# Optimization experiments

Measured on AMD Instinct MI355X. Metric: run time of the kernel, lower is better.

The kernel has to match this reference:

```python
import jax, jax.numpy as jnp
import numpy as np

# Sizes
N, T, P, D = 1000, 4, 10, 13          # nodes, point types, edge types (T*(T+1)/2), basis dim per point
F, H, EA, K, E = 128, 128, 16, 64, 20000  # node feat, edge hidden, edge attr/feat, edge op bottleneck, edges
I_NODE = D * (D + 1) // 2             # 91: symmetric ('ij=ji') self-block irreps dim
I_EDGE = D * D                        # 169: generic ('ij') block irreps dim
AVG_NEIGH = 20.0


def setup_inputs() -> dict:
    ks = jax.random.split(jax.random.key(0), 16)
    Fin = H + 2 * F                   # edge-op input: [edge_msg, node_h_i, node_h_j]
    return {
        'node_feats': jax.random.normal(ks[0], (N, F), jnp.float32),
        'node_attrs': jax.random.uniform(ks[1], (N, T), dtype=jnp.float32),
        'edge_feats': jax.random.normal(ks[2], (E, EA), jnp.float32),
        'edge_attrs': jax.random.normal(ks[3], (E, EA), jnp.float32),
        'edge_index': jax.random.randint(ks[4], (2, E), 0, N),
        'node_types': jax.random.randint(ks[5], (N,), 0, T),
        'edge_types': jax.random.randint(ks[6], (E,), 0, P),
        'W_msg': jax.random.normal(ks[7], (F, F), jnp.float32) / np.float32(np.sqrt(F)),
        'W_attr': jax.random.normal(ks[8], (T, F), jnp.float32) / np.float32(np.sqrt(T)),
        'W_em': jax.random.normal(ks[9], (2 * F + 2 * EA, H), jnp.float32) / np.float32(np.sqrt(2 * F + 2 * EA)),
        'W_proj': jax.random.normal(ks[10], (Fin, K), jnp.float32) / np.float32(np.sqrt(Fin)),
        'W_node': jax.random.normal(ks[11], (T, F, I_NODE), jnp.float32) / np.float32(np.sqrt(F)),
        'W_edge': jax.random.normal(ks[12], (P, K, I_EDGE), jnp.float32) / np.float32(np.sqrt(K)),
        'cob_node': jax.random.normal(ks[13], (T, I_NODE, D, D), jnp.float32) / np.float32(D),
        'cob_edge': jax.random.normal(ks[14], (P, I_EDGE, D, D), jnp.float32) / np.float32(D),
    }


def reference(node_feats, node_attrs, edge_feats, edge_attrs, edge_index, node_types,
              edge_types, W_msg, W_attr, W_em, W_proj, W_node, W_edge, cob_node, cob_edge):
    src, dst = edge_index[0], edge_index[1]
    # --- node message passing (NodeMessageBlock, simplified linear-aggregate form) ---
    m = node_feats @ W_msg                                             # [N, F]
    agg = jax.ops.segment_sum(m[src], dst, num_segments=N) \
        + jax.ops.segment_sum(m[dst], src, num_segments=N)             # symmetric edge list: both dirs
    node_h = node_feats + agg / AVG_NEIGH + node_attrs @ W_attr        # [N, F]
    # --- edge messages (EdgeMessageBlock, simplified) ---
    e_in = jnp.concatenate([node_h[src], node_h[dst], edge_feats, edge_attrs], axis=-1)
    edge_msg = jnp.tanh(e_in @ W_em)                                   # [E, H]
    # --- self-interaction blocks: per-type gather -> op -> einsum('ni,ixy->nxy', ., cob) ---
    node_irred = jnp.einsum('nf,nfi->ni', node_h, W_node[node_types])  # [N, I_NODE]
    node_blocks = jnp.einsum('ni,nixy->nxy', node_irred, cob_node[node_types])  # [N, D, D]
    # --- interaction blocks: per-edge-type op + change of basis, transpose-symmetrized ---
    onehot = jax.nn.one_hot(edge_types, P, dtype=node_feats.dtype)     # [E, P] type selector

    def edge_block(a, b):
        h = jnp.concatenate([edge_msg, a, b], axis=-1) @ W_proj        # [E, K]
        irr = jnp.einsum('epi,ep->ei', jnp.einsum('ek,pki->epi', h, W_edge), onehot)  # [E, I_EDGE]
        return jnp.einsum('epxy,ep->exy', jnp.einsum('ei,pixy->epxy', irr, cob_edge), onehot)  # [E, D, D]

    blk_ij = edge_block(node_h[src], node_h[dst])
    blk_ji = edge_block(node_h[dst], node_h[src])
    edge_blocks = 0.5 * (blk_ij + jnp.swapaxes(blk_ji, -1, -2))        # symm_transpose
    # --- scatter blocks into the dense symmetric block matrix ---
    off = jnp.arange(D)
    nidx = jnp.arange(N)[:, None] * D + off                            # [N, D] diagonal block rows/cols
    rs = src[:, None] * D + off                                        # [E, D]
    cs = dst[:, None] * D + off
    M = jnp.zeros((N * D, N * D), node_feats.dtype)
    M = M.at[nidx[:, :, None], nidx[:, None, :]].add(node_blocks)
    M = M.at[rs[:, :, None], cs[:, None, :]].add(edge_blocks)
    M = M.at[cs[:, :, None], rs[:, None, :]].add(jnp.swapaxes(edge_blocks, -1, -2))
    return M
```

## Files before the change

### kernel.cpp

```cpp
#include <hip/hip_runtime.h>
#include <cmath>

#define NN   1000
#define TT   4
#define PP   10
#define DD   13
#define FF   128
#define HH   128
#define EAA  16
#define KDIM 64
#define EE   20000
#define I_NODE 91
#define I_EDGE 169
#define MROW  13000
#define OUT_FLOAT4 42250000L

__global__ __launch_bounds__(256) void k_zero(float4* __restrict__ p, long n4) {
  long i = (long)blockIdx.x * 256 + threadIdx.x;
  if (i < n4) p[i] = make_float4(0.f, 0.f, 0.f, 0.f);
}

__global__ __launch_bounds__(192) void k_comb_edge(
    const float* __restrict__ We, const float* __restrict__ cob,
    float* __restrict__ Wcomb) {
  int pk = blockIdx.x;
  int p = pk >> 6;
  int t = threadIdx.x;
  if (t >= I_EDGE) return;
  float acc = 0.f;
  const float* wrow = We + pk * I_EDGE;
  const float* crow = cob + p * I_EDGE * I_EDGE + t;
  for (int i = 0; i < I_EDGE; ++i) acc += wrow[i] * crow[i * I_EDGE];
  Wcomb[pk * I_EDGE + t] = acc;
}

__global__ __launch_bounds__(192) void k_comb_node(
    const float* __restrict__ Wn, const float* __restrict__ cob,
    float* __restrict__ Wnc) {
  int tf = blockIdx.x;
  int ty = tf >> 7;
  int t = threadIdx.x;
  if (t >= I_EDGE) return;
  float acc = 0.f;
  const float* wrow = Wn + tf * I_NODE;
  const float* crow = cob + ty * I_NODE * I_EDGE + t;
  for (int i = 0; i < I_NODE; ++i) acc += wrow[i] * crow[i * I_EDGE];
  Wnc[tf * I_EDGE + t] = acc;
}

__global__ __launch_bounds__(128) void k_node_msg(
    const float* __restrict__ nf, const float* __restrict__ Wmsg,
    float* __restrict__ m, float* __restrict__ agg) {
  int n = blockIdx.x, j = threadIdx.x;
  __shared__ float row[FF];
  row[j] = nf[n * FF + j];
  __syncthreads();
  float acc = 0.f;
#pragma unroll 8
  for (int f = 0; f < FF; ++f) acc += row[f] * Wmsg[f * FF + j];
  m[n * FF + j] = acc;
  agg[n * FF + j] = 0.f;
}

__global__ __launch_bounds__(256) void k_scatter(
    const float* __restrict__ m, const int* __restrict__ src,
    const int* __restrict__ dst, float* __restrict__ agg) {
  int idx = blockIdx.x * 256 + threadIdx.x;
  if (idx >= EE * FF) return;
  int e = idx >> 7, j = idx & 127;
  int s = src[e], d = dst[e];
  atomicAdd(&agg[d * FF + j], m[s * FF + j]);
  atomicAdd(&agg[s * FF + j], m[d * FF + j]);
}

__global__ __launch_bounds__(128) void k_node_h(
    const float* __restrict__ nf, const float* __restrict__ agg,
    const float* __restrict__ na, const float* __restrict__ Wattr,
    float* __restrict__ nh) {
  int n = blockIdx.x, j = threadIdx.x;
  float a = 0.f;
#pragma unroll
  for (int t = 0; t < TT; ++t) a += na[n * TT + t] * Wattr[t * FF + j];
  nh[n * FF + j] = nf[n * FF + j] + agg[n * FF + j] * (1.0f / 20.0f) + a;
}

__global__ __launch_bounds__(128) void k_node_pre(
    const float* __restrict__ nh, const float* __restrict__ Wem,
    const float* __restrict__ Wproj, float* __restrict__ V1,
    float* __restrict__ V2, float* __restrict__ U) {
  int n = blockIdx.x, t = threadIdx.x;
  __shared__ float row[FF];
  row[t] = nh[n * FF + t];
  __syncthreads();
  float v1 = 0.f, v2 = 0.f;
#pragma unroll 4
  for (int f = 0; f < FF; ++f) {
    float x = row[f];
    v1 += x * Wem[f * HH + t];
    v2 += x * Wem[(FF + f) * HH + t];
  }
  V1[n * HH + t] = v1;
  V2[n * HH + t] = v2;
  int k = t & 63, half = t >> 6;
  const float* W = Wproj + (FF + half * FF) * KDIM + k;
  float u = 0.f;
#pragma unroll 4
  for (int f = 0; f < FF; ++f) u += row[f] * W[f * KDIM];
  U[n * 128 + t] = u;
}

#define EPB 8
__global__ __launch_bounds__(128) void k_edge_msg(
    const float* __restrict__ V1, const float* __restrict__ V2,
    const float* __restrict__ ef, const float* __restrict__ ea,
    const int* __restrict__ src, const int* __restrict__ dst,
    const float* __restrict__ Wem, const float* __restrict__ Wproj,
    float* __restrict__ hmsg) {
  int e0 = blockIdx.x * EPB;
  int j = threadIdx.x;
  __shared__ float efa[EPB][32];
  __shared__ float em[EPB][HH];
  for (int i = j; i < EPB * 32; i += 128) {
    int e = i >> 5, c = i & 31;
    efa[e][c] = (c < 16) ? ef[(e0 + e) * EAA + c] : ea[(e0 + e) * EAA + (c - 16)];
  }
  __syncthreads();
  float wcol[32];
#pragma unroll
  for (int c = 0; c < 32; ++c) wcol[c] = Wem[(256 + c) * HH + j];
#pragma unroll
  for (int e = 0; e < EPB; ++e) {
    int s = src[e0 + e], d = dst[e0 + e];
    float acc = V1[s * HH + j] + V2[d * HH + j];
#pragma unroll
    for (int c = 0; c < 32; ++c) acc += efa[e][c] * wcol[c];
    em[e][j] = tanhf(acc);
  }
  __syncthreads();
  int k = j & 63, half = j >> 6;
  float a0 = 0.f, a1 = 0.f, a2 = 0.f, a3 = 0.f;
  for (int f = 0; f < HH; f += 4) {
    float4 m0 = *(const float4*)&em[half + 0][f];
    float4 m1 = *(const float4*)&em[half + 2][f];
    float4 m2 = *(const float4*)&em[half + 4][f];
    float4 m3 = *(const float4*)&em[half + 6][f];
    float w0 = Wproj[(f + 0) * KDIM + k], w1 = Wproj[(f + 1) * KDIM + k];
    float w2 = Wproj[(f + 2) * KDIM + k], w3 = Wproj[(f + 3) * KDIM + k];
    a0 += m0.x * w0 + m0.y * w1 + m0.z * w2 + m0.w * w3;
    a1 += m1.x * w0 + m1.y * w1 + m1.z * w2 + m1.w * w3;
    a2 += m2.x * w0 + m2.y * w1 + m2.z * w2 + m2.w * w3;
    a3 += m3.x * w0 + m3.y * w1 + m3.z * w2 + m3.w * w3;
  }
  hmsg[(e0 + half + 0) * KDIM + k] = a0;
  hmsg[(e0 + half + 2) * KDIM + k] = a1;
  hmsg[(e0 + half + 4) * KDIM + k] = a2;
  hmsg[(e0 + half + 6) * KDIM + k] = a3;
}

__global__ __launch_bounds__(192) void k_node_block(
    const float* __restrict__ nh, const int* __restrict__ ntype,
    const float* __restrict__ Wnc, float* __restrict__ M) {
  int n = blockIdx.x, t = threadIdx.x;
  int ty = ntype[n];
  __shared__ float row[FF];
  if (t < FF) row[t] = nh[n * FF + t];
  __syncthreads();
  if (t < I_EDGE) {
    float acc = 0.f;
    const float* W = Wnc + ty * FF * I_EDGE + t;
#pragma unroll 4
    for (int f = 0; f < FF; ++f) acc += row[f] * W[f * I_EDGE];
    int x = t / DD, y = t % DD;
    atomicAdd(&M[(size_t)(n * DD + x) * MROW + (n * DD + y)], acc);
  }
}

#define EB2 4
__global__ __launch_bounds__(768) void k_edge_blk(
    const float* __restrict__ U, const float* __restrict__ hmsg,
    const int* __restrict__ src, const int* __restrict__ dst,
    const int* __restrict__ etype, const float* __restrict__ Wcomb,
    float* __restrict__ M) {
  int e0 = blockIdx.x * EB2;
  int t = threadIdx.x;
  int ei = threadIdx.y;
  int e = e0 + ei;
  __shared__ float h[EB2][2][KDIM];
  __shared__ float tji[EB2][I_EDGE];
  int s = src[e], d = dst[e], p = etype[e];
  if (t < 128) {
    int k = t & 63, w = t >> 6;
    int a = w ? d : s, b = w ? s : d;
    h[ei][w][k] = hmsg[e * KDIM + k] + U[a * 128 + k] + U[b * 128 + 64 + k];
  }
  __syncthreads();
  float bij = 0.f, bji = 0.f;
  if (t < I_EDGE) {
    const float* W = Wcomb + p * KDIM * I_EDGE + t;
    for (int k = 0; k < KDIM; k += 4) {
      float4 hi = *(const float4*)&h[ei][0][k];
      float4 hj = *(const float4*)&h[ei][1][k];
      float w0 = W[(k + 0) * I_EDGE], w1 = W[(k + 1) * I_EDGE];
      float w2 = W[(k + 2) * I_EDGE], w3 = W[(k + 3) * I_EDGE];
      bij += hi.x * w0 + hi.y * w1 + hi.z * w2 + hi.w * w3;
      bji += hj.x * w0 + hj.y * w1 + hj.z * w2 + hj.w * w3;
    }
    tji[ei][t] = bji;
  }
  __syncthreads();
  if (t < I_EDGE) {
    int x = t / DD, y = t % DD;
    float eb = 0.5f * (bij + tji[ei][y * DD + x]);
    atomicAdd(&M[(size_t)(s * DD + x) * MROW + (d * DD + y)], eb);
    atomicAdd(&M[(size_t)(d * DD + y) * MROW + (s * DD + x)], eb);
  }
}

extern "C" void kernel_launch(void* const* d_in, const int* in_sizes, int n_in,
                              void* d_out, int out_size, void* d_ws, size_t ws_size,
                              hipStream_t stream) {
  const float* node_feats = (const float*)d_in[0];
  const float* node_attrs = (const float*)d_in[1];
  const float* edge_feats = (const float*)d_in[2];
  const float* edge_attrs = (const float*)d_in[3];
  const int*   edge_index = (const int*)d_in[4];
  const int*   node_types = (const int*)d_in[5];
  const int*   edge_types = (const int*)d_in[6];
  const float* W_msg  = (const float*)d_in[7];
  const float* W_attr = (const float*)d_in[8];
  const float* W_em   = (const float*)d_in[9];
  const float* W_proj = (const float*)d_in[10];
  const float* W_node = (const float*)d_in[11];
  const float* W_edge = (const float*)d_in[12];
  const float* cob_node = (const float*)d_in[13];
  const float* cob_edge = (const float*)d_in[14];

  float* M  = (float*)d_out;
  float* ws = (float*)d_ws;
  float* m_buf = ws;
  float* agg   = ws + 128000;
  float* nh    = ws + 256000;
  float* V1    = ws + 384000;
  float* V2    = ws + 512000;
  float* U     = ws + 640000;
  float* hmsg  = ws + 768000;
  float* Wcomb = ws + 2048000;
  float* Wnc   = ws + 2156160;

  const int* src = edge_index;
  const int* dst = edge_index + EE;

  k_zero      <<<(int)((OUT_FLOAT4 + 255) / 256), 256, 0, stream>>>((float4*)M, OUT_FLOAT4);
  k_comb_edge <<<PP * KDIM, 192, 0, stream>>>(W_edge, cob_edge, Wcomb);
  k_comb_node <<<TT * FF, 192, 0, stream>>>(W_node, cob_node, Wnc);
  k_node_msg  <<<NN, 128, 0, stream>>>(node_feats, W_msg, m_buf, agg);
  k_scatter   <<<(EE * FF) / 256, 256, 0, stream>>>(m_buf, src, dst, agg);
  k_node_h    <<<NN, 128, 0, stream>>>(node_feats, agg, node_attrs, W_attr, nh);
  k_node_pre  <<<NN, 128, 0, stream>>>(nh, W_em, W_proj, V1, V2, U);
  k_edge_msg  <<<EE / EPB, 128, 0, stream>>>(V1, V2, edge_feats, edge_attrs, src, dst,
                                             W_em, W_proj, hmsg);
  k_node_block<<<NN, 192, 0, stream>>>(nh, node_types, Wnc, M);
  k_edge_blk  <<<dim3(EE / EB2), dim3(192, 4), 0, stream>>>(U, hmsg, src, dst, edge_types,
                                                            Wcomb, M);
}
```

Measured before the change: 892.5 us.

## Fuse setup, node, and edge stages into fewer kernels

Merges the zero-fill, weight-combination and node message kernels into one heterogeneous front kernel that dispatches on block index. The node-h, node-pre and node-block kernels become one per-node kernel, and the edge message MLP moves into the edge-block kernel so the hmsg intermediate is never written to global memory. This cuts launch count and intermediate traffic. In exchange, the edge kernel now recomputes the projection per edge with fewer threads active in its early phases and no register-cached weights.

```diff
diff --git a/kernel.cpp b/kernel.cpp
--- a/kernel.cpp
+++ b/kernel.cpp
@@ -15,51 +15,57 @@
 #define MROW  13000
 #define OUT_FLOAT4 42250000L
 
-__global__ __launch_bounds__(256) void k_zero(float4* __restrict__ p, long n4) {
-  long i = (long)blockIdx.x * 256 + threadIdx.x;
-  if (i < n4) p[i] = make_float4(0.f, 0.f, 0.f, 0.f);
-}
-
-__global__ __launch_bounds__(192) void k_comb_edge(
-    const float* __restrict__ We, const float* __restrict__ cob,
-    float* __restrict__ Wcomb) {
-  int pk = blockIdx.x;
-  int p = pk >> 6;
-  int t = threadIdx.x;
-  if (t >= I_EDGE) return;
-  float acc = 0.f;
-  const float* wrow = We + pk * I_EDGE;
-  const float* crow = cob + p * I_EDGE * I_EDGE + t;
-  for (int i = 0; i < I_EDGE; ++i) acc += wrow[i] * crow[i * I_EDGE];
-  Wcomb[pk * I_EDGE + t] = acc;
-}
-
-__global__ __launch_bounds__(192) void k_comb_node(
-    const float* __restrict__ Wn, const float* __restrict__ cob,
-    float* __restrict__ Wnc) {
-  int tf = blockIdx.x;
-  int ty = tf >> 7;
-  int t = threadIdx.x;
-  if (t >= I_EDGE) return;
-  float acc = 0.f;
-  const float* wrow = Wn + tf * I_NODE;
-  const float* crow = cob + ty * I_NODE * I_EDGE + t;
-  for (int i = 0; i < I_NODE; ++i) acc += wrow[i] * crow[i * I_EDGE];
-  Wnc[tf * I_EDGE + t] = acc;
-}
-
-__global__ __launch_bounds__(128) void k_node_msg(
+#define NB_CE   640
+#define NB_CN   512
+#define NB_MSG  1000
+#define NB_ZERO 8192
+#define NB_FRONT (NB_CE + NB_CN + NB_MSG + NB_ZERO)
+
+__global__ __launch_bounds__(256) void k_front(
+    const float* __restrict__ We, const float* __restrict__ cobE,
+    const float* __restrict__ Wn, const float* __restrict__ cobN,
     const float* __restrict__ nf, const float* __restrict__ Wmsg,
-    float* __restrict__ m, float* __restrict__ agg) {
-  int n = blockIdx.x, j = threadIdx.x;
-  __shared__ float row[FF];
-  row[j] = nf[n * FF + j];
-  __syncthreads();
-  float acc = 0.f;
+    float* __restrict__ Wcomb, float* __restrict__ Wnc,
+    float* __restrict__ m, float* __restrict__ agg,
+    float4* __restrict__ Mz) {
+  int b = blockIdx.x, t = threadIdx.x;
+  if (b < NB_CE) {
+    if (t < I_EDGE) {
+      int pk = b, p = pk >> 6;
+      float acc = 0.f;
+      const float* wrow = We + pk * I_EDGE;
+      const float* crow = cobE + p * I_EDGE * I_EDGE + t;
+      for (int i = 0; i < I_EDGE; ++i) acc += wrow[i] * crow[i * I_EDGE];
+      Wcomb[pk * I_EDGE + t] = acc;
+    }
+  } else if (b < NB_CE + NB_CN) {
+    if (t < I_EDGE) {
+      int tf = b - NB_CE, ty = tf >> 7;
+      float acc = 0.f;
+      const float* wrow = Wn + tf * I_NODE;
+      const float* crow = cobN + ty * I_NODE * I_EDGE + t;
+      for (int i = 0; i < I_NODE; ++i) acc += wrow[i] * crow[i * I_EDGE];
+      Wnc[tf * I_EDGE + t] = acc;
+    }
+  } else if (b < NB_CE + NB_CN + NB_MSG) {
+    int n = b - (NB_CE + NB_CN);
+    __shared__ float row[FF];
+    if (t < FF) row[t] = nf[n * FF + t];
+    __syncthreads();
+    if (t < FF) {
+      float acc = 0.f;
 #pragma unroll 8
-  for (int f = 0; f < FF; ++f) acc += row[f] * Wmsg[f * FF + j];
-  m[n * FF + j] = acc;
-  agg[n * FF + j] = 0.f;
+      for (int f = 0; f < FF; ++f) acc += row[f] * Wmsg[f * FF + t];
+      m[n * FF + t] = acc;
+    } else {
+      agg[n * FF + (t - FF)] = 0.f;
+    }
+  } else {
+    long base = (long)(b - (NB_CE + NB_CN + NB_MSG)) * 256 + t;
+    const long stride = (long)NB_ZERO * 256;
+    float4 z = make_float4(0.f, 0.f, 0.f, 0.f);
+    for (long i = base; i < OUT_FLOAT4; i += stride) Mz[i] = z;
+  }
 }
 
 __global__ __launch_bounds__(256) void k_scatter(
@@ -73,98 +79,42 @@
   atomicAdd(&agg[s * FF + j], m[d * FF + j]);
 }
 
-__global__ __launch_bounds__(128) void k_node_h(
+__global__ __launch_bounds__(192) void k_nodes(
     const float* __restrict__ nf, const float* __restrict__ agg,
     const float* __restrict__ na, const float* __restrict__ Wattr,
-    float* __restrict__ nh) {
-  int n = blockIdx.x, j = threadIdx.x;
-  float a = 0.f;
-#pragma unroll
-  for (int t = 0; t < TT; ++t) a += na[n * TT + t] * Wattr[t * FF + j];
-  nh[n * FF + j] = nf[n * FF + j] + agg[n * FF + j] * (1.0f / 20.0f) + a;
-}
-
-__global__ __launch_bounds__(128) void k_node_pre(
-    const float* __restrict__ nh, const float* __restrict__ Wem,
-    const float* __restrict__ Wproj, float* __restrict__ V1,
-    float* __restrict__ V2, float* __restrict__ U) {
-  int n = blockIdx.x, t = threadIdx.x;
-  __shared__ float row[FF];
-  row[t] = nh[n * FF + t];
-  __syncthreads();
-  float v1 = 0.f, v2 = 0.f;
-#pragma unroll 4
-  for (int f = 0; f < FF; ++f) {
-    float x = row[f];
-    v1 += x * Wem[f * HH + t];
-    v2 += x * Wem[(FF + f) * HH + t];
-  }
-  V1[n * HH + t] = v1;
-  V2[n * HH + t] = v2;
-  int k = t & 63, half = t >> 6;
-  const float* W = Wproj + (FF + half * FF) * KDIM + k;
-  float u = 0.f;
-#pragma unroll 4
-  for (int f = 0; f < FF; ++f) u += row[f] * W[f * KDIM];
-  U[n * 128 + t] = u;
-}
-
-#define EPB 8
-__global__ __launch_bounds__(128) void k_edge_msg(
-    const float* __restrict__ V1, const float* __restrict__ V2,
-    const float* __restrict__ ef, const float* __restrict__ ea,
-    const int* __restrict__ src, const int* __restrict__ dst,
     const float* __restrict__ Wem, const float* __restrict__ Wproj,
-    float* __restrict__ hmsg) {
-  int e0 = blockIdx.x * EPB;
-  int j = threadIdx.x;
-  __shared__ float efa[EPB][32];
-  __shared__ float em[EPB][HH];
-  for (int i = j; i < EPB * 32; i += 128) {
-    int e = i >> 5, c = i & 31;
-    efa[e][c] = (c < 16) ? ef[(e0 + e) * EAA + c] : ea[(e0 + e) * EAA + (c - 16)];
-  }
-  __syncthreads();
-  float wcol[32];
-#pragma unroll
-  for (int c = 0; c < 32; ++c) wcol[c] = Wem[(256 + c) * HH + j];
-#pragma unroll
-  for (int e = 0; e < EPB; ++e) {
-    int s = src[e0 + e], d = dst[e0 + e];
-    float acc = V1[s * HH + j] + V2[d * HH + j];
-#pragma unroll
-    for (int c = 0; c < 32; ++c) acc += efa[e][c] * wcol[c];
-    em[e][j] = tanhf(acc);
-  }
-  __syncthreads();
-  int k = j & 63, half = j >> 6;
-  float a0 = 0.f, a1 = 0.f, a2 = 0.f, a3 = 0.f;
-  for (int f = 0; f < HH; f += 4) {
-    float4 m0 = *(const float4*)&em[half + 0][f];
-    float4 m1 = *(const float4*)&em[half + 2][f];
-    float4 m2 = *(const float4*)&em[half + 4][f];
-    float4 m3 = *(const float4*)&em[half + 6][f];
-    float w0 = Wproj[(f + 0) * KDIM + k], w1 = Wproj[(f + 1) * KDIM + k];
-    float w2 = Wproj[(f + 2) * KDIM + k], w3 = Wproj[(f + 3) * KDIM + k];
-    a0 += m0.x * w0 + m0.y * w1 + m0.z * w2 + m0.w * w3;
-    a1 += m1.x * w0 + m1.y * w1 + m1.z * w2 + m1.w * w3;
-    a2 += m2.x * w0 + m2.y * w1 + m2.z * w2 + m2.w * w3;
-    a3 += m3.x * w0 + m3.y * w1 + m3.z * w2 + m3.w * w3;
-  }
-  hmsg[(e0 + half + 0) * KDIM + k] = a0;
-  hmsg[(e0 + half + 2) * KDIM + k] = a1;
-  hmsg[(e0 + half + 4) * KDIM + k] = a2;
-  hmsg[(e0 + half + 6) * KDIM + k] = a3;
-}
-
-__global__ __launch_bounds__(192) void k_node_block(
-    const float* __restrict__ nh, const int* __restrict__ ntype,
-    const float* __restrict__ Wnc, float* __restrict__ M) {
+    const int* __restrict__ ntype, const float* __restrict__ Wnc,
+    float* __restrict__ nh, float* __restrict__ V1, float* __restrict__ V2,
+    float* __restrict__ U, float* __restrict__ M) {
   int n = blockIdx.x, t = threadIdx.x;
   int ty = ntype[n];
   __shared__ float row[FF];
-  if (t < FF) row[t] = nh[n * FF + t];
-  __syncthreads();
+  if (t < FF) {
+    float a = 0.f;
+#pragma unroll
+    for (int q = 0; q < TT; ++q) a += na[n * TT + q] * Wattr[q * FF + t];
+    float v = nf[n * FF + t] + agg[n * FF + t] * (1.0f / 20.0f) + a;
+    row[t] = v;
+    nh[n * FF + t] = v;
+  }
+  __syncthreads();
+  if (t < FF) {
+    float v1 = 0.f, v2 = 0.f;
+#pragma unroll 4
+    for (int f = 0; f < FF; ++f) {
+      float x = row[f];
+      v1 += x * Wem[f * HH + t];
+      v2 += x * Wem[(FF + f) * HH + t];
+    }
+    V1[n * HH + t] = v1;
+    V2[n * HH + t] = v2;
+    int k = t & 63, half = t >> 6;
+    const float* W = Wproj + (FF + half * FF) * KDIM + k;
+    float u = 0.f;
+#pragma unroll 4
+    for (int f = 0; f < FF; ++f) u += row[f] * W[f * KDIM];
+    U[n * 128 + t] = u;
+  }
   if (t < I_EDGE) {
     float acc = 0.f;
     const float* W = Wnc + ty * FF * I_EDGE + t;
@@ -175,25 +125,46 @@
   }
 }
 
-#define EB2 4
-__global__ __launch_bounds__(768) void k_edge_blk(
-    const float* __restrict__ U, const float* __restrict__ hmsg,
-    const int* __restrict__ src, const int* __restrict__ dst,
-    const int* __restrict__ etype, const float* __restrict__ Wcomb,
-    float* __restrict__ M) {
-  int e0 = blockIdx.x * EB2;
+#define EB 4
+__global__ __launch_bounds__(768) void k_edge_all(
+    const float* __restrict__ V1, const float* __restrict__ V2,
+    const float* __restrict__ U, const float* __restrict__ ef,
+    const float* __restrict__ ea, const int* __restrict__ src,
+    const int* __restrict__ dst, const int* __restrict__ etype,
+    const float* __restrict__ Wem, const float* __restrict__ Wproj,
+    const float* __restrict__ Wcomb, float* __restrict__ M) {
   int t = threadIdx.x;
   int ei = threadIdx.y;
-  int e = e0 + ei;
-  __shared__ float h[EB2][2][KDIM];
-  __shared__ float tji[EB2][I_EDGE];
+  int e = blockIdx.x * EB + ei;
   int s = src[e], d = dst[e], p = etype[e];
-  if (t < 128) {
-    int k = t & 63, w = t >> 6;
-    int a = w ? d : s, b = w ? s : d;
-    h[ei][w][k] = hmsg[e * KDIM + k] + U[a * 128 + k] + U[b * 128 + 64 + k];
-  }
-  __syncthreads();
+  __shared__ __align__(16) float efa[EB][32];
+  __shared__ __align__(16) float em[EB][HH];
+  __shared__ __align__(16) float h[EB][2][KDIM];
+  __shared__ __align__(16) float tji[EB][I_EDGE];
+
+  if (t < 32) efa[ei][t] = (t < 16) ? ef[e * EAA + t] : ea[e * EAA + (t - 16)];
+  __syncthreads();
+
+  if (t < HH) {
+    float acc = V1[s * HH + t] + V2[d * HH + t];
+#pragma unroll
+    for (int c = 0; c < 32; ++c) acc += efa[ei][c] * Wem[(256 + c) * HH + t];
+    em[ei][t] = tanhf(acc);
+  }
+  __syncthreads();
+
+  if (t < KDIM) {
+    float hm = 0.f;
+    for (int f = 0; f < HH; f += 4) {
+      float4 mv = *(const float4*)&em[ei][f];
+      hm += mv.x * Wproj[(f + 0) * KDIM + t] + mv.y * Wproj[(f + 1) * KDIM + t]
+          + mv.z * Wproj[(f + 2) * KDIM + t] + mv.w * Wproj[(f + 3) * KDIM + t];
+    }
+    h[ei][0][t] = hm + U[s * 128 + t] + U[d * 128 + 64 + t];
+    h[ei][1][t] = hm + U[d * 128 + t] + U[s * 128 + 64 + t];
+  }
+  __syncthreads();
+
   float bij = 0.f, bji = 0.f;
   if (t < I_EDGE) {
     const float* W = Wcomb + p * KDIM * I_EDGE + t;
@@ -243,23 +214,21 @@
   float* V1    = ws + 384000;
   float* V2    = ws + 512000;
   float* U     = ws + 640000;
-  float* hmsg  = ws + 768000;
-  float* Wcomb = ws + 2048000;
-  float* Wnc   = ws + 2156160;
+  float* Wcomb = ws + 768000;
+  float* Wnc   = ws + 876160;
 
   const int* src = edge_index;
   const int* dst = edge_index + EE;
 
-  k_zero      <<<(int)((OUT_FLOAT4 + 255) / 256), 256, 0, stream>>>((float4*)M, OUT_FLOAT4);
-  k_comb_edge <<<PP * KDIM, 192, 0, stream>>>(W_edge, cob_edge, Wcomb);
-  k_comb_node <<<TT * FF, 192, 0, stream>>>(W_node, cob_node, Wnc);
-  k_node_msg  <<<NN, 128, 0, stream>>>(node_feats, W_msg, m_buf, agg);
-  k_scatter   <<<(EE * FF) / 256, 256, 0, stream>>>(m_buf, src, dst, agg);
-  k_node_h    <<<NN, 128, 0, stream>>>(node_feats, agg, node_attrs, W_attr, nh);
-  k_node_pre  <<<NN, 128, 0, stream>>>(nh, W_em, W_proj, V1, V2, U);
-  k_edge_msg  <<<EE / EPB, 128, 0, stream>>>(V1, V2, edge_feats, edge_attrs, src, dst,
-                                             W_em, W_proj, hmsg);
-  k_node_block<<<NN, 192, 0, stream>>>(nh, node_types, Wnc, M);
-  k_edge_blk  <<<dim3(EE / EB2), dim3(192, 4), 0, stream>>>(U, hmsg, src, dst, edge_types,
-                                                            Wcomb, M);
-}
+  k_front   <<<NB_FRONT, 256, 0, stream>>>(W_edge, cob_edge, W_node, cob_node,
+                                           node_feats, W_msg, Wcomb, Wnc,
+                                           m_buf, agg, (float4*)M);
+  k_scatter <<<(EE * FF) / 256, 256, 0, stream>>>(m_buf, src, dst, agg);
+  k_nodes   <<<NN, 192, 0, stream>>>(node_feats, agg, node_attrs, W_attr,
+                                     W_em, W_proj, node_types, Wnc,
+                                     nh, V1, V2, U, M);
+  k_edge_all<<<dim3(EE / EB), dim3(192, 4), 0, stream>>>(V1, V2, U, edge_feats,
+                                                         edge_attrs, src, dst,
+                                                         edge_types, W_em, W_proj,
+                                                         Wcomb, M);
+}
```

Result: slower. 940.3 us (+5.4%).

## Merge small kernels into fewer launches and overlap output zeroing with scatter

Applied to the files above, without the earlier changes.

Combines the weight-combination kernels and the node message GEMM into a single multi-role launch. The 676 MB output zero-fill now shares a launch with the atomic scatter of node messages, using a grid-stride loop over 8192 blocks. The node_h, node_pre and node_block kernels become one per-node kernel that keeps node_h in shared memory instead of writing it out and reading it back. The goal is to cut launch overhead and global round trips. The cost is that role-divergent blocks of different lengths share one grid, and the zero-fill now runs on a fixed block count rather than one thread per float4.

```diff
diff --git a/kernel.cpp b/kernel.cpp
--- a/kernel.cpp
+++ b/kernel.cpp
@@ -15,98 +15,125 @@
 #define MROW  13000
 #define OUT_FLOAT4 42250000L
 
-__global__ __launch_bounds__(256) void k_zero(float4* __restrict__ p, long n4) {
-  long i = (long)blockIdx.x * 256 + threadIdx.x;
-  if (i < n4) p[i] = make_float4(0.f, 0.f, 0.f, 0.f);
-}
-
-__global__ __launch_bounds__(192) void k_comb_edge(
-    const float* __restrict__ We, const float* __restrict__ cob,
-    float* __restrict__ Wcomb) {
-  int pk = blockIdx.x;
-  int p = pk >> 6;
-  int t = threadIdx.x;
-  if (t >= I_EDGE) return;
-  float acc = 0.f;
-  const float* wrow = We + pk * I_EDGE;
-  const float* crow = cob + p * I_EDGE * I_EDGE + t;
-  for (int i = 0; i < I_EDGE; ++i) acc += wrow[i] * crow[i * I_EDGE];
-  Wcomb[pk * I_EDGE + t] = acc;
-}
-
-__global__ __launch_bounds__(192) void k_comb_node(
-    const float* __restrict__ Wn, const float* __restrict__ cob,
-    float* __restrict__ Wnc) {
-  int tf = blockIdx.x;
-  int ty = tf >> 7;
-  int t = threadIdx.x;
-  if (t >= I_EDGE) return;
-  float acc = 0.f;
-  const float* wrow = Wn + tf * I_NODE;
-  const float* crow = cob + ty * I_NODE * I_EDGE + t;
-  for (int i = 0; i < I_NODE; ++i) acc += wrow[i] * crow[i * I_EDGE];
-  Wnc[tf * I_EDGE + t] = acc;
-}
-
-__global__ __launch_bounds__(128) void k_node_msg(
+#define WS_M     0L
+#define WS_AGG   128000L
+#define WS_V1    256000L
+#define WS_V2    384000L
+#define WS_U     512000L
+#define WS_HMSG  640000L
+#define WS_WCOMB 1920000L
+#define WS_WNC   2028160L
+
+#define NB_CE   640
+#define NB_CN   512
+#define NB_MSG  1000
+#define NB_FRONT (NB_CE + NB_CN + NB_MSG)
+
+__global__ __launch_bounds__(256) void k_front(
+    const float* __restrict__ We, const float* __restrict__ cobE,
+    const float* __restrict__ Wn, const float* __restrict__ cobN,
     const float* __restrict__ nf, const float* __restrict__ Wmsg,
+    float* __restrict__ Wcomb, float* __restrict__ Wnc,
     float* __restrict__ m, float* __restrict__ agg) {
-  int n = blockIdx.x, j = threadIdx.x;
-  __shared__ float row[FF];
-  row[j] = nf[n * FF + j];
-  __syncthreads();
-  float acc = 0.f;
+  int b = blockIdx.x, t = threadIdx.x;
+  if (b < NB_CE) {
+    if (t < I_EDGE) {
+      int pk = b, p = pk >> 6;
+      float acc = 0.f;
+      const float* wrow = We + pk * I_EDGE;
+      const float* crow = cobE + p * I_EDGE * I_EDGE + t;
+      for (int i = 0; i < I_EDGE; ++i) acc += wrow[i] * crow[i * I_EDGE];
+      Wcomb[pk * I_EDGE + t] = acc;
+    }
+  } else if (b < NB_CE + NB_CN) {
+    if (t < I_EDGE) {
+      int tf = b - NB_CE, ty = tf >> 7;
+      float acc = 0.f;
+      const float* wrow = Wn + tf * I_NODE;
+      const float* crow = cobN + ty * I_NODE * I_EDGE + t;
+      for (int i = 0; i < I_NODE; ++i) acc += wrow[i] * crow[i * I_EDGE];
+      Wnc[tf * I_EDGE + t] = acc;
+    }
+  } else {
+    int n = b - (NB_CE + NB_CN);
+    __shared__ float row[FF];
+    if (t < FF) row[t] = nf[n * FF + t];
+    __syncthreads();
+    if (t < FF) {
+      float acc = 0.f;
 #pragma unroll 8
-  for (int f = 0; f < FF; ++f) acc += row[f] * Wmsg[f * FF + j];
-  m[n * FF + j] = acc;
-  agg[n * FF + j] = 0.f;
-}
-
-__global__ __launch_bounds__(256) void k_scatter(
-    const float* __restrict__ m, const int* __restrict__ src,
-    const int* __restrict__ dst, float* __restrict__ agg) {
-  int idx = blockIdx.x * 256 + threadIdx.x;
-  if (idx >= EE * FF) return;
-  int e = idx >> 7, j = idx & 127;
-  int s = src[e], d = dst[e];
-  atomicAdd(&agg[d * FF + j], m[s * FF + j]);
-  atomicAdd(&agg[s * FF + j], m[d * FF + j]);
-}
-
-__global__ __launch_bounds__(128) void k_node_h(
+      for (int f = 0; f < FF; ++f) acc += row[f] * Wmsg[f * FF + t];
+      m[n * FF + t] = acc;
+    } else {
+      agg[n * FF + (t - FF)] = 0.f;
+    }
+  }
+}
+
+#define NB_Z 8192
+#define NB_SC ((EE * FF) / 256)
+
+__global__ __launch_bounds__(256) void k_zero_scatter(
+    float4* __restrict__ Mz, const float* __restrict__ m,
+    const int* __restrict__ src, const int* __restrict__ dst,
+    float* __restrict__ agg) {
+  int b = blockIdx.x, t = threadIdx.x;
+  if (b < NB_Z) {
+    long base = (long)b * 256 + t;
+    const long stride = (long)NB_Z * 256;
+    const float4 z = make_float4(0.f, 0.f, 0.f, 0.f);
+    for (long i = base; i < OUT_FLOAT4; i += stride) Mz[i] = z;
+  } else {
+    int idx = (b - NB_Z) * 256 + t;
+    int e = idx >> 7, j = idx & 127;
+    int s = src[e], d = dst[e];
+    atomicAdd(&agg[d * FF + j], m[s * FF + j]);
+    atomicAdd(&agg[s * FF + j], m[d * FF + j]);
+  }
+}
+
+__global__ __launch_bounds__(192) void k_nodes(
     const float* __restrict__ nf, const float* __restrict__ agg,
     const float* __restrict__ na, const float* __restrict__ Wattr,
-    float* __restrict__ nh) {
-  int n = blockIdx.x, j = threadIdx.x;
-  float a = 0.f;
-#pragma unroll
-  for (int t = 0; t < TT; ++t) a += na[n * TT + t] * Wattr[t * FF + j];
-  nh[n * FF + j] = nf[n * FF + j] + agg[n * FF + j] * (1.0f / 20.0f) + a;
-}
-
-__global__ __launch_bounds__(128) void k_node_pre(
-    const float* __restrict__ nh, const float* __restrict__ Wem,
-    const float* __restrict__ Wproj, float* __restrict__ V1,
-    float* __restrict__ V2, float* __restrict__ U) {
+    const float* __restrict__ Wem, const float* __restrict__ Wproj,
+    const int* __restrict__ ntype, const float* __restrict__ Wnc,
+    float* __restrict__ V1, float* __restrict__ V2, float* __restrict__ U,
+    float* __restrict__ M) {
   int n = blockIdx.x, t = threadIdx.x;
+  int ty = ntype[n];
   __shared__ float row[FF];
-  row[t] = nh[n * FF + t];
-  __syncthreads();
-  float v1 = 0.f, v2 = 0.f;
+  if (t < FF) {
+    float a = 0.f;
+#pragma unroll
+    for (int q = 0; q < TT; ++q) a += na[n * TT + q] * Wattr[q * FF + t];
+    row[t] = nf[n * FF + t] + agg[n * FF + t] * (1.0f / 20.0f) + a;
+  }
+  __syncthreads();
+  if (t < FF) {
+    float v1 = 0.f, v2 = 0.f;
 #pragma unroll 4
-  for (int f = 0; f < FF; ++f) {
-    float x = row[f];
-    v1 += x * Wem[f * HH + t];
-    v2 += x * Wem[(FF + f) * HH + t];
-  }
-  V1[n * HH + t] = v1;
-  V2[n * HH + t] = v2;
-  int k = t & 63, half = t >> 6;
-  const float* W = Wproj + (FF + half * FF) * KDIM + k;
-  float u = 0.f;
+    for (int f = 0; f < FF; ++f) {
+      float x = row[f];
+      v1 += x * Wem[f * HH + t];
+      v2 += x * Wem[(FF + f) * HH + t];
+    }
+    V1[n * HH + t] = v1;
+    V2[n * HH + t] = v2;
+    int k = t & 63, half = t >> 6;
+    const float* W = Wproj + (FF + half * FF) * KDIM + k;
+    float u = 0.f;
 #pragma unroll 4
-  for (int f = 0; f < FF; ++f) u += row[f] * W[f * KDIM];
-  U[n * 128 + t] = u;
+    for (int f = 0; f < FF; ++f) u += row[f] * W[f * KDIM];
+    U[n * 128 + t] = u;
+  }
+  if (t < I_EDGE) {
+    float acc = 0.f;
+    const float* W = Wnc + ty * FF * I_EDGE + t;
+#pragma unroll 4
+    for (int f = 0; f < FF; ++f) acc += row[f] * W[f * I_EDGE];
+    int x = t / DD, y = t % DD;
+    atomicAdd(&M[(size_t)(n * DD + x) * MROW + (n * DD + y)], acc);
+  }
 }
 
 #define EPB 8
@@ -157,37 +184,18 @@
   hmsg[(e0 + half + 6) * KDIM + k] = a3;
 }
 
-__global__ __launch_bounds__(192) void k_node_block(
-    const float* __restrict__ nh, const int* __restrict__ ntype,
-    const float* __restrict__ Wnc, float* __restrict__ M) {
-  int n = blockIdx.x, t = threadIdx.x;
-  int ty = ntype[n];
-  __shared__ float row[FF];
-  if (t < FF) row[t] = nh[n * FF + t];
-  __syncthreads();
-  if (t < I_EDGE) {
-    float acc = 0.f;
-    const float* W = Wnc + ty * FF * I_EDGE + t;
-#pragma unroll 4
-    for (int f = 0; f < FF; ++f) acc += row[f] * W[f * I_EDGE];
-    int x = t / DD, y = t % DD;
-    atomicAdd(&M[(size_t)(n * DD + x) * MROW + (n * DD + y)], acc);
-  }
-}
-
 #define EB2 4
 __global__ __launch_bounds__(768) void k_edge_blk(
     const float* __restrict__ U, const float* __restrict__ hmsg,
     const int* __restrict__ src, const int* __restrict__ dst,
     const int* __restrict__ etype, const float* __restrict__ Wcomb,
     float* __restrict__ M) {
-  int e0 = blockIdx.x * EB2;
   int t = threadIdx.x;
   int ei = threadIdx.y;
-  int e = e0 + ei;
-  __shared__ float h[EB2][2][KDIM];
-  __shared__ float tji[EB2][I_EDGE];
+  int e = blockIdx.x * EB2 + ei;
   int s = src[e], d = dst[e], p = etype[e];
+  __shared__ __align__(16) float h[EB2][2][KDIM];
+  __shared__ __align__(16) float tji[EB2][I_EDGE];
   if (t < 128) {
     int k = t & 63, w = t >> 6;
     int a = w ? d : s, b = w ? s : d;
@@ -237,29 +245,27 @@
 
   float* M  = (float*)d_out;
   float* ws = (float*)d_ws;
-  float* m_buf = ws;
-  float* agg   = ws + 128000;
-  float* nh    = ws + 256000;
-  float* V1    = ws + 384000;
-  float* V2    = ws + 512000;
-  float* U     = ws + 640000;
-  float* hmsg  = ws + 768000;
-  float* Wcomb = ws + 2048000;
-  float* Wnc   = ws + 2156160;
+  float* m_buf = ws + WS_M;
+  float* agg   = ws + WS_AGG;
+  float* V1    = ws + WS_V1;
+  float* V2    = ws + WS_V2;
+  float* U     = ws + WS_U;
+  float* hmsg  = ws + WS_HMSG;
+  float* Wcomb = ws + WS_WCOMB;
+  float* Wnc   = ws + WS_WNC;
 
   const int* src = edge_index;
   const int* dst = edge_index + EE;
 
-  k_zero      <<<(int)((OUT_FLOAT4 + 255) / 256), 256, 0, stream>>>((float4*)M, OUT_FLOAT4);
-  k_comb_edge <<<PP * KDIM, 192, 0, stream>>>(W_edge, cob_edge, Wcomb);
-  k_comb_node <<<TT * FF, 192, 0, stream>>>(W_node, cob_node, Wnc);
-  k_node_msg  <<<NN, 128, 0, stream>>>(node_feats, W_msg, m_buf, agg);
-  k_scatter   <<<(EE * FF) / 256, 256, 0, stream>>>(m_buf, src, dst, agg);
-  k_node_h    <<<NN, 128, 0, stream>>>(node_feats, agg, node_attrs, W_attr, nh);
-  k_node_pre  <<<NN, 128, 0, stream>>>(nh, W_em, W_proj, V1, V2, U);
-  k_edge_msg  <<<EE / EPB, 128, 0, stream>>>(V1, V2, edge_feats, edge_attrs, src, dst,
-                                             W_em, W_proj, hmsg);
-  k_node_block<<<NN, 192, 0, stream>>>(nh, node_types, Wnc, M);
-  k_edge_blk  <<<dim3(EE / EB2), dim3(192, 4), 0, stream>>>(U, hmsg, src, dst, edge_types,
-                                                            Wcomb, M);
-}
+  k_front       <<<NB_FRONT, 256, 0, stream>>>(W_edge, cob_edge, W_node, cob_node,
+                                               node_feats, W_msg, Wcomb, Wnc,
+                                               m_buf, agg);
+  k_zero_scatter<<<NB_Z + NB_SC, 256, 0, stream>>>((float4*)M, m_buf, src, dst, agg);
+  k_nodes       <<<NN, 192, 0, stream>>>(node_feats, agg, node_attrs, W_attr,
+                                         W_em, W_proj, node_types, Wnc,
+                                         V1, V2, U, M);
+  k_edge_msg    <<<EE / EPB, 128, 0, stream>>>(V1, V2, edge_feats, edge_attrs,
+                                               src, dst, W_em, W_proj, hmsg);
+  k_edge_blk    <<<dim3(EE / EB2), dim3(192, 4), 0, stream>>>(U, hmsg, src, dst,
+                                                              edge_types, Wcomb, M);
+}
```

New measurement: 917.4 us. 2.8% more time.
